# Kernel tuning notes

Measured on AMD Instinct MI355X. Metric: run time of the kernel, lower is better.

Reference implementation:

```python
import math
import jax
import jax.numpy as jnp
import numpy as np
from jax import lax

B_, L, D_MODEL = 2, 1024, 2048
D_STATE, D_CONV, EXPAND = 16, 4, 2
D_INNER = EXPAND * D_MODEL          # 4096
DT_RANK = math.ceil(D_MODEL / 16)   # 128


def setup_inputs() -> dict:
    key = jax.random.key(0)
    ks = jax.random.split(key, 8)
    hidden_states = jax.random.normal(ks[0], (B_, L, D_MODEL), jnp.float32)
    in_proj_w = jax.random.normal(ks[1], (2 * D_INNER, D_MODEL), jnp.float32) * (D_MODEL ** -0.5)
    conv_w = jax.random.normal(ks[2], (D_INNER, D_CONV), jnp.float32) * (D_CONV ** -0.5)
    conv_b = jnp.zeros((D_INNER,), jnp.float32)
    x_proj_w = jax.random.normal(ks[3], (DT_RANK + 2 * D_STATE, D_INNER), jnp.float32) * (D_INNER ** -0.5)
    dt_std = DT_RANK ** -0.5
    dt_proj_w = jax.random.uniform(ks[4], (D_INNER, DT_RANK), jnp.float32, minval=-dt_std, maxval=dt_std)
    # dt bias init: softplus^{-1} of dt sampled log-uniform in [1e-3, 1e-1]
    dt = jnp.exp(jax.random.uniform(ks[5], (D_INNER,), jnp.float32)
                 * (math.log(0.1) - math.log(0.001)) + math.log(0.001))
    dt = jnp.clip(dt, 1e-4)
    dt_proj_b = dt + jnp.log(-jnp.expm1(-dt))
    A_log = jnp.log(jnp.broadcast_to(jnp.arange(1, D_STATE + 1, dtype=jnp.float32), (D_INNER, D_STATE)))
    D = jnp.ones((D_INNER,), jnp.float32)
    out_proj_w = jax.random.normal(ks[6], (D_MODEL, D_INNER), jnp.float32) * (D_INNER ** -0.5)
    return {
        'hidden_states': hidden_states, 'in_proj_w': in_proj_w,
        'conv_w': conv_w, 'conv_b': conv_b, 'x_proj_w': x_proj_w,
        'dt_proj_w': dt_proj_w, 'dt_proj_b': dt_proj_b,
        'A_log': A_log, 'D': D, 'out_proj_w': out_proj_w,
    }


def _silu(v):
    return v * jax.nn.sigmoid(v)


def _mamba_forward(hidden_states, in_proj_w, conv_w, conv_b, x_proj_w,
                   dt_proj_w, dt_proj_b, A_log, D, out_proj_w):
    b, l, _ = hidden_states.shape
    # in_proj: (b,l,d_model) -> (b, 2*d_inner, l)
    xz = jnp.einsum('bld,ed->bel', hidden_states, in_proj_w)
    x, z = xz[:, :D_INNER, :], xz[:, D_INNER:, :]
    A = -jnp.exp(A_log.astype(jnp.float32))  # (d_inner, d_state)
    # causal depthwise conv1d + SiLU
    xp = jnp.pad(x, ((0, 0), (0, 0), (D_CONV - 1, 0)))
    x = lax.conv_general_dilated(
        xp, conv_w[:, None, :], window_strides=(1,), padding='VALID',
        dimension_numbers=('NCH', 'OIH', 'NCH'), feature_group_count=D_INNER)
    x = _silu(x + conv_b[None, :, None])  # (b, d_inner, l)
    # x_proj -> dt, B, C
    x_dbl = jnp.einsum('bdl,kd->blk', x, x_proj_w)  # (b,l,dt_rank+2n)
    dt_lo = x_dbl[..., :DT_RANK]
    Bmat = x_dbl[..., DT_RANK:DT_RANK + D_STATE]          # (b,l,n)
    Cmat = x_dbl[..., DT_RANK + D_STATE:]                 # (b,l,n)
    delta = jax.nn.softplus(jnp.einsum('blr,dr->bld', dt_lo, dt_proj_w)
                            + dt_proj_b.astype(jnp.float32))  # (b,l,d)
    xt = jnp.transpose(x, (2, 0, 1))       # (l,b,d)
    dl = jnp.transpose(delta, (1, 0, 2))   # (l,b,d)
    Bl = jnp.transpose(Bmat, (1, 0, 2))    # (l,b,n)
    Cl = jnp.transpose(Cmat, (1, 0, 2))    # (l,b,n)

    def step(h, inp):
        d_t, B_t, C_t, x_t = inp
        dA = jnp.exp(d_t[..., None] * A)                       # (b,d,n)
        h = h * dA + d_t[..., None] * B_t[:, None, :] * x_t[..., None]
        y_t = jnp.sum(h * C_t[:, None, :], axis=-1)            # (b,d)
        return h, y_t

    h0 = jnp.zeros((b, D_INNER, D_STATE), jnp.float32)
    _, ys = lax.scan(step, h0, (dl, Bl, Cl, xt))  # ys: (l,b,d)
    y = jnp.transpose(ys, (1, 0, 2))              # (b,l,d)
    y = y + jnp.transpose(x, (0, 2, 1)) * D[None, None, :]
    y = y * _silu(jnp.transpose(z, (0, 2, 1)))
    out = jnp.einsum('bld,ed->ble', y, out_proj_w)  # (b,l,d_model)
    return out


def reference(hidden_states, in_proj_w, conv_w, conv_b, x_proj_w,
              dt_proj_w, dt_proj_b, A_log, D, out_proj_w):
    return _mamba_forward(hidden_states, in_proj_w, conv_w, conv_b, x_proj_w,
                          dt_proj_w, dt_proj_b, A_log, D, out_proj_w)
```

## Files before the change

### kernel.cpp

```cpp
#include <hip/hip_runtime.h>
#include <hip/hip_bf16.h>
#include <stdint.h>

#define BB 2
#define LL 1024
#define DMODEL 2048
#define DINNER 4096
#define DSTATE 16
#define DTRANK 128
#define XDBL_LD 256
#define CHUNK 64
#define NCH (LL / CHUNK)

typedef unsigned short ushort;
using short8 = __attribute__((ext_vector_type(8))) short;
using f32x4  = __attribute__((ext_vector_type(4))) float;
using us4    = __attribute__((ext_vector_type(4))) ushort;

__device__ __forceinline__ float bf2f(ushort u) {
    union { uint32_t i; float f; } v; v.i = ((uint32_t)u) << 16; return v.f;
}
__device__ __forceinline__ ushort f2bf(float f) {
    union { float f; uint32_t i; } v; v.f = f;
    uint32_t lsb = (v.i >> 16) & 1u;
    uint32_t r = v.i + 0x7FFFu + lsb;
    return (ushort)(r >> 16);
}

__device__ __forceinline__ void glds16(const ushort* g, ushort* l) {
    __builtin_amdgcn_global_load_lds(
        (const __attribute__((address_space(1))) void*)g,
        (__attribute__((address_space(3))) void*)l,
        16, 0, 0);
}

__global__ __launch_bounds__(256) void cvt_all(
    const float4* __restrict__ hidden, const float4* __restrict__ inproj,
    const float4* __restrict__ dtw, const float4* __restrict__ outp,
    const float4* __restrict__ xproj,
    us4* __restrict__ hid_h, us4* __restrict__ inp_h, us4* __restrict__ dtp_h,
    us4* __restrict__ outp_h, us4* __restrict__ xpp)
{
    long i = (long)blockIdx.x * 256 + threadIdx.x;
    const float4* src; us4* dst; long j;
    if (i < 1048576)      { src = hidden; dst = hid_h;  j = i; }
    else if (i < 5242880) { src = inproj; dst = inp_h;  j = i - 1048576; }
    else if (i < 5373952) { src = dtw;    dst = dtp_h;  j = i - 5242880; }
    else if (i < 7471104) { src = outp;   dst = outp_h; j = i - 5373952; }
    else {
        j = i - 7471104; dst = xpp;
        if (j >= 163840) { us4 z = {0, 0, 0, 0}; dst[j] = z; return; }
        src = xproj;
    }
    float4 v = src[j];
    us4 o; o.x = f2bf(v.x); o.y = f2bf(v.y); o.z = f2bf(v.z); o.w = f2bf(v.w);
    dst[j] = o;
}

template <bool WF, bool WH>
__global__ __launch_bounds__(512, 2) void gemm_nt256(
    const ushort* __restrict__ A, int lda,
    const ushort* __restrict__ Bm, int ldb,
    float* __restrict__ Cf, ushort* __restrict__ Ch, int ldc,
    int K)
{
    __shared__ __align__(16) ushort sA[2][256 * 64];
    __shared__ __align__(16) ushort sB[2][256 * 64];

    const int tid  = threadIdx.x;
    const int lane = tid & 63;
    const int wave = tid >> 6;
    const int wr   = wave >> 2;
    const int wcol = wave & 3;
    const int lrow = lane & 15;
    const int lg   = lane >> 4;
    const int s7   = lane & 7;
    const int kb0 = ((0 + lg) ^ s7) << 4;
    const int kb1 = ((4 + lg) ^ s7) << 4;

    const int NT = gridDim.x, MT = gridDim.y;
    int mt, nt;
    if ((NT & 7) == 0) {
        int lin   = blockIdx.y * NT + blockIdx.x;
        int strip = NT >> 3;
        int xcd   = lin & 7;
        int idx   = lin >> 3;
        nt = xcd * strip + (idx % strip);
        mt = idx / strip;
    } else { mt = blockIdx.y; nt = blockIdx.x; }
    const long m0 = (long)mt * 256;
    const long n0 = (long)nt * 256;

    const long zoff = (long)blockIdx.z;
    A  += zoff * (long)K;
    Bm += zoff * (long)K;
    const long Mrows = (long)MT * 256;
    if (WF) Cf += zoff * Mrows * (long)ldc;

    f32x4 acc[8][4] = {};

    const int sr   = tid >> 3;
    const int scol = (((tid & 7) ^ (sr & 7)) << 3);
    const ushort* Ag = A  + (m0 + sr) * (long)lda + scol;
    const ushort* Bg = Bm + (n0 + sr) * (long)ldb + scol;

    const int NKT = K >> 6;

    {
        ushort* dA0 = &sA[0][0] + tid * 8;
        ushort* dB0 = &sB[0][0] + tid * 8;
        #pragma unroll
        for (int c = 0; c < 4; ++c) {
            glds16(Ag + (c * 64) * (long)lda, dA0 + c * 4096);
            glds16(Bg + (c * 64) * (long)ldb, dB0 + c * 4096);
        }
    }
    __syncthreads();

    const int arow0 = (wr * 128 + lrow) * 128;
    const int brow0 = (wcol * 64 + lrow) * 128;

    for (int kt = 0; kt < NKT; ++kt) {
        const int p = kt & 1;
        const char* sap = (const char*)&sA[p][0];
        const char* sbp = (const char*)&sB[p][0];
        ushort* dA = &sA[p ^ 1][0] + tid * 8;
        ushort* dB = &sB[p ^ 1][0] + tid * 8;
        const long knext = (long)(kt + 1) << 6;
        const bool pf = (kt + 1 < NKT);

        #pragma unroll
        for (int mh = 0; mh < 2; ++mh) {
            short8 af[4][2];
            #pragma unroll
            for (int i4 = 0; i4 < 4; ++i4) {
                const int ab = arow0 + (mh * 64 + i4 * 16) * 128;
                af[i4][0] = *(const short8*)(sap + ab + kb0);
                af[i4][1] = *(const short8*)(sap + ab + kb1);
            }
            #pragma unroll
            for (int nh = 0; nh < 2; ++nh) {
                short8 bf[2][2];
                #pragma unroll
                for (int j2 = 0; j2 < 2; ++j2) {
                    const int bb = brow0 + (nh * 32 + j2 * 16) * 128;
                    bf[j2][0] = *(const short8*)(sbp + bb + kb0);
                    bf[j2][1] = *(const short8*)(sbp + bb + kb1);
                }
                if (pf && mh == 0) {
                    if (nh == 0) {
                        #pragma unroll
                        for (int c = 0; c < 4; ++c)
                            glds16(Ag + (c * 64) * (long)lda + knext,
                                   dA + c * 4096);
                    } else {
                        #pragma unroll
                        for (int c = 0; c < 4; ++c)
                            glds16(Bg + (c * 64) * (long)ldb + knext,
                                   dB + c * 4096);
                    }
                }
                __builtin_amdgcn_s_setprio(1);
                #pragma unroll
                for (int ks = 0; ks < 2; ++ks)
                    #pragma unroll
                    for (int i4 = 0; i4 < 4; ++i4)
                        #pragma unroll
                        for (int j2 = 0; j2 < 2; ++j2)
                            acc[mh * 4 + i4][nh * 2 + j2] =
                                __builtin_amdgcn_mfma_f32_16x16x32_bf16(
                                    af[i4][ks], bf[j2][ks],
                                    acc[mh * 4 + i4][nh * 2 + j2], 0, 0, 0);
                __builtin_amdgcn_s_setprio(0);
            }
        }
        __syncthreads();
    }

    const int r0 = (lane >> 4) * 4;
    const int c0 = lane & 15;
    #pragma unroll
    for (int i = 0; i < 8; ++i) {
        #pragma unroll
        for (int j = 0; j < 4; ++j) {
            const long col = n0 + wcol * 64 + j * 16 + c0;
            #pragma unroll
            for (int r = 0; r < 4; ++r) {
                const long row = m0 + wr * 128 + i * 16 + r0 + r;
                const float v = acc[i][j][r];
                const long idx = row * (long)ldc + col;
                if (WF) Cf[idx] = v;
                if (WH) Ch[idx] = f2bf(v);
            }
        }
    }
}

template <int EPI, bool WF, bool WH>
__global__ __launch_bounds__(256) void gemm_nt(
    const ushort* __restrict__ A, int lda,
    const ushort* __restrict__ Bm, int ldb,
    float* __restrict__ Cf, ushort* __restrict__ Ch, int ldc,
    int K, const float* __restrict__ bias)
{
    __shared__ __align__(16) ushort sA[128 * 64];
    __shared__ __align__(16) ushort sB[128 * 64];

    const int tid  = threadIdx.x;
    const int lane = tid & 63;
    const int wave = tid >> 6;
    const int wr = wave >> 1, wc = wave & 1;

    const int NT = gridDim.x, MT = gridDim.y;
    int mt, nt;
    if ((NT & 7) == 0) {
        int lin   = blockIdx.y * NT + blockIdx.x;
        int strip = NT >> 3;
        int xcd   = lin & 7;
        int idx   = lin >> 3;
        nt = xcd * strip + (idx % strip);
        mt = idx / strip;
    } else { mt = blockIdx.y; nt = blockIdx.x; }
    const long m0 = (long)mt * 128;
    const long n0 = (long)nt * 128;

    const long zoff = (long)blockIdx.z;
    A  += zoff * (long)K;
    Bm += zoff * (long)K;
    const long Mrows = (long)MT * 128;
    if (WF) Cf += zoff * Mrows * (long)ldc;
    if (WH) Ch += zoff * Mrows * (long)ldc;

    f32x4 acc[4][4] = {};

    const int lrow = lane & 15;
    const int lko  = (lane >> 4) << 3;

    const int sr = tid >> 3;
    const int sc = (tid & 7) << 3;
    const ushort* Ag = A  + (m0 + sr) * (long)lda + sc;
    const ushort* Bg = Bm + (n0 + sr) * (long)ldb + sc;
    ushort* lA = sA + tid * 8;
    ushort* lB = sB + tid * 8;

    for (int k0 = 0; k0 < K; k0 += 64) {
        __syncthreads();
        #pragma unroll
        for (int c = 0; c < 4; ++c) {
            glds16(Ag + (c * 32) * (long)lda + k0, lA + c * 2048);
            glds16(Bg + (c * 32) * (long)ldb + k0, lB + c * 2048);
        }
        __syncthreads();

        #pragma unroll
        for (int ks = 0; ks < 2; ++ks) {
            short8 af[4], bf[4];
            #pragma unroll
            for (int i = 0; i < 4; ++i)
                af[i] = *(const short8*)&sA[(wr * 64 + i * 16 + lrow) * 64 + ks * 32 + lko];
            #pragma unroll
            for (int j = 0; j < 4; ++j)
                bf[j] = *(const short8*)&sB[(wc * 64 + j * 16 + lrow) * 64 + ks * 32 + lko];

            #pragma unroll
            for (int i = 0; i < 4; ++i)
                #pragma unroll
                for (int j = 0; j < 4; ++j)
                    acc[i][j] = __builtin_amdgcn_mfma_f32_16x16x32_bf16(
                        af[i], bf[j], acc[i][j], 0, 0, 0);
        }
    }

    const int r0 = (lane >> 4) * 4;
    const int c0 = lane & 15;
    #pragma unroll
    for (int i = 0; i < 4; ++i) {
        #pragma unroll
        for (int j = 0; j < 4; ++j) {
            long col = n0 + wc * 64 + j * 16 + c0;
            float bv = 0.f;
            if (EPI == 1) bv = bias[col];
            #pragma unroll
            for (int r = 0; r < 4; ++r) {
                long row = m0 + wr * 64 + i * 16 + r0 + r;
                float v = acc[i][j][r];
                if (EPI == 1) {
                    v += bv;
                    v = (v > 20.f) ? v : log1pf(__expf(v));
                }
                long idx = row * (long)ldc + col;
                if (WF) Cf[idx] = v;
                if (WH) Ch[idx] = f2bf(v);
            }
        }
    }
}

template <int NZ, bool WH_>
__global__ __launch_bounds__(256) void reduce_k(
    const float4* __restrict__ parts, long stride4, int n4,
    float4* __restrict__ outF, us4* __restrict__ outH)
{
    int i = blockIdx.x * 256 + threadIdx.x;
    if (i >= n4) return;
    float4 s = parts[i];
    #pragma unroll
    for (int z = 1; z < NZ; ++z) {
        float4 v = parts[(long)z * stride4 + i];
        s.x += v.x; s.y += v.y; s.z += v.z; s.w += v.w;
    }
    if (outF) outF[i] = s;
    if (WH_) {
        us4 o; o.x = f2bf(s.x); o.y = f2bf(s.y); o.z = f2bf(s.z); o.w = f2bf(s.w);
        outH[i] = o;
    }
}

__global__ __launch_bounds__(256) void conv_silu_kernel(
    const ushort* __restrict__ xz,
    const float* __restrict__ cw,
    const float* __restrict__ cb,
    ushort* __restrict__ xc)
{
    int gid = blockIdx.x * 256 + threadIdx.x;
    int d  = gid & (DINNER - 1);
    int rl = gid >> 12;
    int l  = rl & (LL - 1);
    float acc = cb[d];
    #pragma unroll
    for (int j = 0; j < 4; ++j) {
        int li = l - 3 + j;
        if (li >= 0)
            acc += cw[d * 4 + j] * bf2f(xz[(long)(rl - 3 + j) * 8192 + d]);
    }
    float s = acc / (1.f + __expf(-acc));
    xc[gid] = f2bf(s);
}

__global__ __launch_bounds__(256) void scan_p1(
    const ushort* __restrict__ delta,
    const ushort* __restrict__ xc,
    const float*  __restrict__ xdbl,
    const float*  __restrict__ A_log,
    float* __restrict__ Hbuf,
    float* __restrict__ sumdt_buf)
{
    __shared__ float sB[CHUNK * 16];
    const int tid = threadIdx.x;
    const int k = blockIdx.y, b = blockIdx.z;
    const int d = blockIdx.x * 256 + tid;
    const int row0 = b * LL + k * CHUNK;

    #pragma unroll
    for (int i = 0; i < 4; ++i) {
        int idx = i * 256 + tid;
        sB[idx] = xdbl[(long)(row0 + (idx >> 4)) * XDBL_LD + DTRANK + (idx & 15)];
    }
    __syncthreads();

    float A[DSTATE];
    const float4* Ap = (const float4*)(A_log + d * DSTATE);
    #pragma unroll
    for (int i = 0; i < 4; ++i) {
        float4 v = Ap[i];
        A[i*4+0] = -__expf(v.x); A[i*4+1] = -__expf(v.y);
        A[i*4+2] = -__expf(v.z); A[i*4+3] = -__expf(v.w);
    }

    float H[DSTATE];
    #pragma unroll
    for (int s = 0; s < DSTATE; ++s) H[s] = 0.f;
    float sumdt = 0.f;

    for (int t = 0; t < CHUNK; ++t) {
        const long row = row0 + t;
        const float dt = bf2f(delta[row * DINNER + d]);
        const float xv = bf2f(xc[row * DINNER + d]);
        const float dx = dt * xv;
        sumdt += dt;
        #pragma unroll
        for (int s = 0; s < DSTATE; ++s) {
            float dA = __expf(dt * A[s]);
            H[s] = H[s] * dA + dx * sB[t * 16 + s];
        }
    }

    const long o = ((long)(b * NCH + k) * DINNER + d) * DSTATE;
    float4* Ho = (float4*)(Hbuf + o);
    #pragma unroll
    for (int i = 0; i < 4; ++i) {
        float4 v; v.x = H[i*4+0]; v.y = H[i*4+1]; v.z = H[i*4+2]; v.w = H[i*4+3];
        Ho[i] = v;
    }
    sumdt_buf[(b * NCH + k) * DINNER + d] = sumdt;
}

__global__ __launch_bounds__(256) void scan_p2(
    const float* __restrict__ A_log,
    const float* __restrict__ sumdt_buf,
    float* __restrict__ Hbuf)
{
    int gid = blockIdx.x * 256 + threadIdx.x;
    int b = gid >> 16;
    int rem = gid & 65535;
    int d = rem >> 4, s = rem & 15;
    float A = -__expf(A_log[d * DSTATE + s]);
    float h = 0.f;
    for (int k = 0; k < NCH; ++k) {
        long idx = ((long)(b * NCH + k) * DINNER + d) * DSTATE + s;
        float Hk = Hbuf[idx];
        float sd = sumdt_buf[(b * NCH + k) * DINNER + d];
        Hbuf[idx] = h;
        h = h * __expf(A * sd) + Hk;
    }
}

__global__ __launch_bounds__(256) void scan_p3(
    const ushort* __restrict__ delta,
    const ushort* __restrict__ xc,
    const float*  __restrict__ xdbl,
    const ushort* __restrict__ xz,
    const float*  __restrict__ A_log,
    const float*  __restrict__ Dp,
    const float*  __restrict__ hin,
    ushort* __restrict__ y)
{
    __shared__ float sBC[CHUNK * 32];
    const int tid = threadIdx.x;
    const int k = blockIdx.y, b = blockIdx.z;
    const int d = blockIdx.x * 256 + tid;
    const int row0 = b * LL + k * CHUNK;

    #pragma unroll
    for (int i = 0; i < 8; ++i) {
        int idx = i * 256 + tid;
        sBC[idx] = xdbl[(long)(row0 + (idx >> 5)) * XDBL_LD + DTRANK + (idx & 31)];
    }
    __syncthreads();

    float A[DSTATE];
    const float4* Ap = (const float4*)(A_log + d * DSTATE);
    #pragma unroll
    for (int i = 0; i < 4; ++i) {
        float4 v = Ap[i];
        A[i*4+0] = -__expf(v.x); A[i*4+1] = -__expf(v.y);
        A[i*4+2] = -__expf(v.z); A[i*4+3] = -__expf(v.w);
    }
    const float Dd = Dp[d];

    float h[DSTATE];
    const float4* Hp = (const float4*)(hin + ((long)(b * NCH + k) * DINNER + d) * DSTATE);
    #pragma unroll
    for (int i = 0; i < 4; ++i) {
        float4 v = Hp[i];
        h[i*4+0] = v.x; h[i*4+1] = v.y; h[i*4+2] = v.z; h[i*4+3] = v.w;
    }

    for (int t = 0; t < CHUNK; ++t) {
        const long row = row0 + t;
        const float dt = bf2f(delta[row * DINNER + d]);
        const float xv = bf2f(xc[row * DINNER + d]);
        const float dx = dt * xv;
        float yt = 0.f;
        #pragma unroll
        for (int s = 0; s < DSTATE; ++s) {
            float dA = __expf(dt * A[s]);
            h[s] = h[s] * dA + dx * sBC[t * 32 + s];
            yt += h[s] * sBC[t * 32 + 16 + s];
        }
        yt += xv * Dd;
        const float zv = bf2f(xz[row * 8192 + DINNER + d]);
        yt *= zv / (1.f + __expf(-zv));
        y[row * DINNER + d] = f2bf(yt);
    }
}

extern "C" void kernel_launch(void* const* d_in, const int* in_sizes, int n_in,
                              void* d_out, int out_size, void* d_ws, size_t ws_size,
                              hipStream_t stream)
{
    const float* hidden    = (const float*)d_in[0];
    const float* in_proj   = (const float*)d_in[1];
    const float* conv_w    = (const float*)d_in[2];
    const float* conv_b    = (const float*)d_in[3];
    const float* x_proj    = (const float*)d_in[4];
    const float* dt_proj_w = (const float*)d_in[5];
    const float* dt_proj_b = (const float*)d_in[6];
    const float* A_log     = (const float*)d_in[7];
    const float* Dp        = (const float*)d_in[8];
    const float* out_proj  = (const float*)d_in[9];
    float* out = (float*)d_out;

    char* ws = (char*)d_ws;
    ushort* xz_h    = (ushort*)(ws);
    ushort* xc      = (ushort*)(ws + 33554432);
    ushort* xpp     = (ushort*)(ws + 50331648);
    float*  xdbl    = (float*)(ws + 52428800);
    ushort* xdblh   = (ushort*)(ws + 54525952);
    ushort* delta_h = (ushort*)(ws + 55574528);
    ushort* yb      = (ushort*)(ws + 72351744);
    ushort* hid_h   = (ushort*)(ws + 89128960);
    ushort* inp_h   = (ushort*)(ws + 97517568);
    float*  parts   = (float*)(ws + 97517568);
    float*  Hbuf    = (float*)(ws + 97517568);
    float*  sumdt   = (float*)(ws + 105906176);
    ushort* dtp_h   = (ushort*)(ws + 131072000);
    ushort* outp_h  = (ushort*)(ws + 132120576);
    float*  parts2  = (float*)(ws);

    const int M = BB * LL;

    cvt_all<<<30208, 256, 0, stream>>>(
        (const float4*)hidden, (const float4*)in_proj, (const float4*)dt_proj_w,
        (const float4*)out_proj, (const float4*)x_proj,
        (us4*)hid_h, (us4*)inp_h, (us4*)dtp_h, (us4*)outp_h, (us4*)xpp);

    gemm_nt256<false, true><<<dim3(8192 / 256, M / 256), 512, 0, stream>>>(
        hid_h, DMODEL, inp_h, DMODEL, nullptr, xz_h, 8192, DMODEL);

    conv_silu_kernel<<<(M * DINNER) / 256, 256, 0, stream>>>(xz_h, conv_w, conv_b, xc);

    gemm_nt<0, true, false><<<dim3(XDBL_LD / 128, M / 128, 16), 256, 0, stream>>>(
        xc, DINNER, xpp, DINNER, parts, nullptr, XDBL_LD, DINNER / 16, nullptr);
    reduce_k<16, true><<<(M * XDBL_LD / 4 + 255) / 256, 256, 0, stream>>>(
        (const float4*)parts, (long)M * XDBL_LD / 4, M * XDBL_LD / 4,
        (float4*)xdbl, (us4*)xdblh);

    gemm_nt<1, false, true><<<dim3(DINNER / 128, M / 128), 256, 0, stream>>>(
        xdblh, XDBL_LD, dtp_h, DTRANK, nullptr, delta_h, DINNER, DTRANK, dt_proj_b);

    scan_p1<<<dim3(DINNER / 256, NCH, BB), 256, 0, stream>>>(
        delta_h, xc, xdbl, A_log, Hbuf, sumdt);
    scan_p2<<<(BB * DINNER * DSTATE) / 256, 256, 0, stream>>>(
        A_log, sumdt, Hbuf);
    scan_p3<<<dim3(DINNER / 256, NCH, BB), 256, 0, stream>>>(
        delta_h, xc, xdbl, xz_h, A_log, Dp, Hbuf, yb);

    gemm_nt256<true, false><<<dim3(DMODEL / 256, M / 256, 4), 512, 0, stream>>>(
        yb, DINNER, outp_h, DINNER, parts2, nullptr, DMODEL, DINNER / 4);
    reduce_k<4, false><<<(M * DMODEL / 4 + 255) / 256, 256, 0, stream>>>(
        (const float4*)parts2, (long)M * DMODEL / 4, M * DMODEL / 4,
        (float4*)out, nullptr);
}
```

Before: 449.1 us.

## Split GEMM k-step into four phases with staged prefetch and explicit vmcnt waits

```diff
diff --git a/kernel.cpp b/kernel.cpp
--- a/kernel.cpp
+++ b/kernel.cpp
@@ -33,6 +33,9 @@
         (__attribute__((address_space(3))) void*)l,
         16, 0, 0);
 }
+
+#define BAR() __builtin_amdgcn_s_barrier()
+#define WAITV(n) asm volatile("s_waitcnt vmcnt(" #n ")" ::: "memory")
 
 __global__ __launch_bounds__(256) void cvt_all(
     const float4* __restrict__ hidden, const float4* __restrict__ inproj,
@@ -101,80 +104,99 @@
 
     const int sr   = tid >> 3;
     const int scol = (((tid & 7) ^ (sr & 7)) << 3);
-    const ushort* Ag = A  + (m0 + sr) * (long)lda + scol;
-    const ushort* Bg = Bm + (n0 + sr) * (long)ldb + scol;
+    const ushort* Ag = A + (m0 + sr) * (long)lda + scol;
+    const int brow_s = ((sr >> 5) << 6) + (sr & 31);
+    const ushort* BgS = Bm + (n0 + brow_s) * (long)ldb + scol;
 
     const int NKT = K >> 6;
 
-    {
-        ushort* dA0 = &sA[0][0] + tid * 8;
-        ushort* dB0 = &sB[0][0] + tid * 8;
-        #pragma unroll
-        for (int c = 0; c < 4; ++c) {
-            glds16(Ag + (c * 64) * (long)lda, dA0 + c * 4096);
-            glds16(Bg + (c * 64) * (long)ldb, dB0 + c * 4096);
-        }
-    }
-    __syncthreads();
-
     const int arow0 = (wr * 128 + lrow) * 128;
-    const int brow0 = (wcol * 64 + lrow) * 128;
+    const int brow0 = (wcol >> 1) * 8192 + (((wcol & 1) << 5) + lrow) * 128;
+
+    short8 af[4][2], bf[2][2];
+
+    auto readA = [&](const char* sap, int mh) {
+        const int ab = arow0 + mh * (64 * 128);
+        #pragma unroll
+        for (int i4 = 0; i4 < 4; ++i4) {
+            af[i4][0] = *(const short8*)(sap + ab + i4 * (16 * 128) + kb0);
+            af[i4][1] = *(const short8*)(sap + ab + i4 * (16 * 128) + kb1);
+        }
+    };
+    auto readB = [&](const char* sbp, int nh) {
+        const int bb = brow0 + nh * 16384;
+        #pragma unroll
+        for (int j2 = 0; j2 < 2; ++j2) {
+            bf[j2][0] = *(const short8*)(sbp + bb + j2 * (16 * 128) + kb0);
+            bf[j2][1] = *(const short8*)(sbp + bb + j2 * (16 * 128) + kb1);
+        }
+    };
+    auto stageA = [&](int h, ushort* dst, long koff) {
+        glds16(Ag + (h * 64) * (long)lda + koff,        dst + h * 4096 + tid * 8);
+        glds16(Ag + (h * 64 + 128) * (long)lda + koff,  dst + (h + 2) * 4096 + tid * 8);
+    };
+    auto stageB = [&](int h, ushort* dst, long koff) {
+        glds16(BgS + (32 * h) * (long)ldb + koff,       dst + (2 * h) * 4096 + tid * 8);
+        glds16(BgS + (128 + 32 * h) * (long)ldb + koff, dst + (2 * h + 1) * 4096 + tid * 8);
+    };
+    auto mfma16 = [&](int mh, int nh) {
+        __builtin_amdgcn_s_setprio(1);
+        #pragma unroll
+        for (int ks = 0; ks < 2; ++ks)
+            #pragma unroll
+            for (int i4 = 0; i4 < 4; ++i4)
+                #pragma unroll
+                for (int j2 = 0; j2 < 2; ++j2)
+                    acc[mh * 4 + i4][nh * 2 + j2] =
+                        __builtin_amdgcn_mfma_f32_16x16x32_bf16(
+                            af[i4][ks], bf[j2][ks],
+                            acc[mh * 4 + i4][nh * 2 + j2], 0, 0, 0);
+        __builtin_amdgcn_s_setprio(0);
+    };
+
+    stageA(0, &sA[0][0], 0);
+    stageB(0, &sB[0][0], 0);
+    stageB(1, &sB[0][0], 0);
+    stageA(1, &sA[0][0], 0);
+    WAITV(4);
+    BAR();
 
     for (int kt = 0; kt < NKT; ++kt) {
-        const int p = kt & 1;
-        const char* sap = (const char*)&sA[p][0];
-        const char* sbp = (const char*)&sB[p][0];
-        ushort* dA = &sA[p ^ 1][0] + tid * 8;
-        ushort* dB = &sB[p ^ 1][0] + tid * 8;
-        const long knext = (long)(kt + 1) << 6;
+        const char* sap = (const char*)&sA[kt & 1][0];
+        const char* sbp = (const char*)&sB[kt & 1][0];
+        ushort* dAn = &sA[(kt & 1) ^ 1][0];
+        ushort* dBn = &sB[(kt & 1) ^ 1][0];
+        const long kn = (long)(kt + 1) << 6;
         const bool pf = (kt + 1 < NKT);
 
-        #pragma unroll
-        for (int mh = 0; mh < 2; ++mh) {
-            short8 af[4][2];
-            #pragma unroll
-            for (int i4 = 0; i4 < 4; ++i4) {
-                const int ab = arow0 + (mh * 64 + i4 * 16) * 128;
-                af[i4][0] = *(const short8*)(sap + ab + kb0);
-                af[i4][1] = *(const short8*)(sap + ab + kb1);
-            }
-            #pragma unroll
-            for (int nh = 0; nh < 2; ++nh) {
-                short8 bf[2][2];
-                #pragma unroll
-                for (int j2 = 0; j2 < 2; ++j2) {
-                    const int bb = brow0 + (nh * 32 + j2 * 16) * 128;
-                    bf[j2][0] = *(const short8*)(sbp + bb + kb0);
-                    bf[j2][1] = *(const short8*)(sbp + bb + kb1);
-                }
-                if (pf && mh == 0) {
-                    if (nh == 0) {
-                        #pragma unroll
-                        for (int c = 0; c < 4; ++c)
-                            glds16(Ag + (c * 64) * (long)lda + knext,
-                                   dA + c * 4096);
-                    } else {
-                        #pragma unroll
-                        for (int c = 0; c < 4; ++c)
-                            glds16(Bg + (c * 64) * (long)ldb + knext,
-                                   dB + c * 4096);
-                    }
-                }
-                __builtin_amdgcn_s_setprio(1);
-                #pragma unroll
-                for (int ks = 0; ks < 2; ++ks)
-                    #pragma unroll
-                    for (int i4 = 0; i4 < 4; ++i4)
-                        #pragma unroll
-                        for (int j2 = 0; j2 < 2; ++j2)
-                            acc[mh * 4 + i4][nh * 2 + j2] =
-                                __builtin_amdgcn_mfma_f32_16x16x32_bf16(
-                                    af[i4][ks], bf[j2][ks],
-                                    acc[mh * 4 + i4][nh * 2 + j2], 0, 0, 0);
-                __builtin_amdgcn_s_setprio(0);
-            }
-        }
-        __syncthreads();
+        readA(sap, 0);
+        readB(sbp, 0);
+        if (pf) stageA(0, dAn, kn);
+        BAR();
+        mfma16(0, 0);
+        if (pf) { WAITV(4); } else { WAITV(2); }
+        BAR();
+
+        readB(sbp, 1);
+        if (pf) stageB(0, dBn, kn);
+        BAR();
+        mfma16(0, 1);
+        if (pf) { WAITV(4); } else { WAITV(0); }
+        BAR();
+
+        readA(sap, 1);
+        readB(sbp, 0);
+        if (pf) stageB(1, dBn, kn);
+        BAR();
+        mfma16(1, 0);
+        BAR();
+
+        readB(sbp, 1);
+        if (pf) stageA(1, dAn, kn);
+        BAR();
+        mfma16(1, 1);
+        if (pf) { WAITV(4); }
+        BAR();
     }
 
     const int r0 = (lane >> 4) * 4;
```

Result: slower. 463.1 us (+3.1%).
